# Kernel optimization log

Hardware: AMD Instinct MI355X
Metric: run time of the kernel (lower is better)

Reference implementation:

```python
import jax, jax.numpy as jnp
import numpy as np

KERNEL_MUL = 2.0
KERNEL_NUM = 5


def setup_inputs() -> dict:
    key = jax.random.key(0)
    k1, k2 = jax.random.split(key)
    N, D = 4096, 256
    source = jax.random.normal(k1, (N, D), dtype=jnp.float32)
    target = jax.random.normal(k2, (N, D), dtype=jnp.float32)
    return {"source": source, "target": target}


def _gaussian_kernel_sum(source, target):
    # total: [2N, D]
    total = jnp.concatenate([source, target], axis=0)
    n = total.shape[0]
    sq = jnp.sum(total * total, axis=1)  # [2N]
    L2 = sq[:, None] + sq[None, :] - 2.0 * (total @ total.T)  # [2N, 2N]
    # Bandwidth from detached mean of off-diagonal-normalized sum (torch uses .data)
    bandwidth = jax.lax.stop_gradient(jnp.sum(L2)) / (n * n - n)
    bandwidth = bandwidth / (KERNEL_MUL ** (KERNEL_NUM // 2))
    kernels = sum(
        jnp.exp(-L2 / (bandwidth * (KERNEL_MUL ** i))) for i in range(KERNEL_NUM)
    )
    return kernels


def reference(source, target):
    b = source.shape[0]
    K = _gaussian_kernel_sum(source, target)
    XX = jnp.mean(K[:b, :b])
    YY = jnp.mean(K[b:, b:])
    XY = jnp.mean(K[:b, b:])
    YX = jnp.mean(K[b:, :b])
    return XX + YY - XY - YX
```

## Files before the change

kernel.cpp:

```cpp
#include <hip/hip_runtime.h>


#define NROWS 8192
#define HALF  4096
#define DIM   256
#define CONVB 256
#define NTILE 2080
#define GRIDP 512

typedef float f32x4 __attribute__((ext_vector_type(4)));
typedef float f32x2 __attribute__((ext_vector_type(2)));

__device__ __forceinline__ const float* row_ptr(const float* src, const float* tgt, int r) {
    return (r < HALF) ? (src + (size_t)r * DIM) : (tgt + (size_t)(r - HALF) * DIM);
}

__device__ __forceinline__ void gload_lds16(const void* g, void* l) {
    __builtin_amdgcn_global_load_lds(
        (const __attribute__((address_space(1))) unsigned int*)g,
        (__attribute__((address_space(3))) unsigned int*)l, 16, 0, 0);
}

__device__ __forceinline__ void stage_panel(const ulonglong2* plane, int P,
                                            ulonglong2* lds, int w, int lane) {
    #pragma unroll
    for (int i = 0; i < 8; ++i) {
        int k = w + 4 * i;
        int u = k >> 1;
        int h = k & 1;
        int rg = (h * 64 + lane) ^ ((u & 3) << 1);
        gload_lds16(plane + (size_t)P * 2048 + (size_t)u * 128 + rg,
                    lds + u * 128 + h * 64);
    }
}

__global__ __launch_bounds__(256) void k_conv(const float* __restrict__ src,
                                              const float* __restrict__ tgt,
                                              unsigned char* __restrict__ hi,
                                              float* __restrict__ sq,
                                              float* __restrict__ part,
                                              double* __restrict__ parts1,
                                              float* __restrict__ out) {
    __shared__ __align__(16) unsigned char sh8[32 * 256];
    __shared__ float4 cs[4][64];
    __shared__ double s1s[4];

    int w = threadIdx.x >> 6, lane = threadIdx.x & 63;
    int r0 = blockIdx.x * 32;

    float4 v[8];
    #pragma unroll
    for (int i = 0; i < 8; ++i) {
        int row = r0 + w * 8 + i;
        v[i] = ((const float4*)row_ptr(src, tgt, row))[lane];
    }

    float4 csum = {0.f, 0.f, 0.f, 0.f};
    double s1w = 0.0;
    #pragma unroll
    for (int i = 0; i < 8; ++i) {
        int rl  = w * 8 + i;
        float xs[4] = {v[i].x, v[i].y, v[i].z, v[i].w};
        int pk = __builtin_amdgcn_cvt_pk_fp8_f32(xs[0], xs[1], 0, false);
        pk     = __builtin_amdgcn_cvt_pk_fp8_f32(xs[2], xs[3], pk, true);
        int o  = lane >> 1, h = lane & 1;
        *(int*)&sh8[rl * 256 + (((o ^ rl) & 31) << 3) + (h << 2)] = pk;
        csum.x += xs[0]; csum.y += xs[1]; csum.z += xs[2]; csum.w += xs[3];
        float sf = xs[0]*xs[0] + xs[1]*xs[1] + xs[2]*xs[2] + xs[3]*xs[3];
        float q0 = __builtin_amdgcn_cvt_f32_fp8(pk, 0);
        float q1 = __builtin_amdgcn_cvt_f32_fp8(pk, 1);
        float q2 = __builtin_amdgcn_cvt_f32_fp8(pk, 2);
        float q3 = __builtin_amdgcn_cvt_f32_fp8(pk, 3);
        float sQ = q0*q0 + q1*q1 + q2*q2 + q3*q3;
        #pragma unroll
        for (int off = 32; off; off >>= 1) {
            sf += __shfl_xor(sf, off, 64);
            sQ += __shfl_xor(sQ, off, 64);
        }
        if (lane == 0) { sq[r0 + rl] = sQ; s1w += (double)sf; }
    }
    __syncthreads();
    int panel = blockIdx.x >> 2, quarter = blockIdx.x & 3;
    #pragma unroll
    for (int c = threadIdx.x; c < 512; c += 256) {
        int u = c >> 5, rl = c & 31;
        int tt = u >> 2, j = u & 3;
        int o0 = 8 * tt + j;
        int o1 = 8 * tt + 4 + j;
        unsigned long long q0 = *(const unsigned long long*)
            &sh8[rl * 256 + (((o0 ^ rl) & 31) << 3)];
        unsigned long long q1 = *(const unsigned long long*)
            &sh8[rl * 256 + (((o1 ^ rl) & 31) << 3)];
        ulonglong2 q = {q0, q1};
        size_t goff = ((size_t)panel * 2048 + (size_t)u * 128 + quarter * 32 + rl);
        ((ulonglong2*)hi)[goff] = q;
    }
    cs[w][lane] = csum;
    if (lane == 0) s1s[w] = s1w;
    __syncthreads();
    if (w == 0) {
        float4 a = cs[0][lane], b = cs[1][lane], c = cs[2][lane], d = cs[3][lane];
        float4 tot = {a.x + b.x + c.x + d.x, a.y + b.y + c.y + d.y,
                      a.z + b.z + c.z + d.z, a.w + b.w + c.w + d.w};
        *(float4*)&part[(size_t)blockIdx.x * DIM + lane * 4] = tot;
        if (lane == 0) parts1[blockIdx.x] = s1s[0] + s1s[1] + s1s[2] + s1s[3];
    }
    if (blockIdx.x == 0 && threadIdx.x == 0) out[0] = 0.0f;
}

__global__ __launch_bounds__(256) void k_scale(const double* __restrict__ parts1,
                                               const float* __restrict__ part,
                                               float* __restrict__ scale) {
    __shared__ double sh[256];
    int t = threadIdx.x;
    sh[t] = parts1[t];
    __syncthreads();
    for (int off = 128; off; off >>= 1) {
        if (t < off) sh[t] += sh[t + off];
        __syncthreads();
    }
    double S1 = sh[0];
    __syncthreads();
    float c0 = 0.f, c1 = 0.f, c2 = 0.f, c3 = 0.f;
    #pragma unroll 16
    for (int b = 0; b < CONVB; b += 4) {
        c0 += part[(b + 0) * DIM + t];
        c1 += part[(b + 1) * DIM + t];
        c2 += part[(b + 2) * DIM + t];
        c3 += part[(b + 3) * DIM + t];
    }
    double c = (double)((c0 + c1) + (c2 + c3));
    sh[t] = c * c;
    __syncthreads();
    for (int off = 128; off; off >>= 1) {
        if (t < off) sh[t] += sh[t + off];
        __syncthreads();
    }
    if (t == 0) {
        double S2    = sh[0];
        double n     = (double)NROWS;
        double sumL2 = 2.0 * n * S1 - 2.0 * S2;
        double bw    = sumL2 / (n * n - n) / 4.0;
        *scale = (float)(-1.0 / (16.0 * bw * 0.69314718055994530942));
    }
}

__global__ __launch_bounds__(256, 2) void k_pairs(const unsigned char* __restrict__ hi,
                                                  const float* __restrict__ sq,
                                                  const float* __restrict__ scale_p,
                                                  float* __restrict__ pb) {
    __shared__ __align__(16) ulonglong2 ldsA[2048];
    __shared__ __align__(16) ulonglong2 ldsB[2048];
    __shared__ float wsum[4];

    int bid = blockIdx.x;
    int t0 = (bid * NTILE) / GRIDP;
    int t1 = ((bid + 1) * NTILE) / GRIDP;

    int id = t0, I = 0;
    for (;;) {
        int c = 64 - I;
        if (id < c) break;
        id -= c; ++I;
    }
    int J = I + id;

    int t    = threadIdx.x;
    int lane = t & 63;
    int w    = t >> 6;
    int lr   = lane & 15, lq = lane >> 4;
    int wr   = w >> 1, wc = w & 1;
    int lrx  = lr ^ (lq << 1);

    const ulonglong2* plane = (const ulonglong2*)hi;
    float s = *scale_p;
    f32x2 m2s = {-2.0f * s, -2.0f * s};

    stage_panel(plane, I, ldsA, w, lane);
    if (J != I) stage_panel(plane, J, ldsB, w, lane);
    asm volatile("s_waitcnt vmcnt(0)");
    __syncthreads();

    float wtot = 0.0f;
    int curI = I, curJ = J;

    #pragma unroll 1
    for (int tile = t0; tile < t1; ++tile) {
        const ulonglong2* lB  = (curJ == curI) ? ldsA : ldsB;
        const ulonglong2* pAl = ldsA + lq * 128 + wr * 64 + lrx;
        const ulonglong2* pBl = lB   + lq * 128 + wc * 64 + lrx;

        ulonglong2 fA[4][4], fB[4][4];
        #pragma unroll
        for (int tt = 0; tt < 4; ++tt) {
            #pragma unroll
            for (int m = 0; m < 4; ++m) fA[tt][m] = pAl[tt * 512 + m * 16];
            #pragma unroll
            for (int n = 0; n < 4; ++n) fB[tt][n] = pBl[tt * 512 + n * 16];
        }
        __syncthreads();

        int nI = curI, nJ = curJ + 1;
        if (nJ == 64) { nI = curI + 1; nJ = nI; }
        if (tile + 1 < t1) {
            if (nI != curI) stage_panel(plane, nI, ldsA, w, lane);
            else            stage_panel(plane, nJ, ldsB, w, lane);
        }

        f32x4 acc[4][4];
        #pragma unroll
        for (int m = 0; m < 4; ++m)
            #pragma unroll
            for (int n = 0; n < 4; ++n) acc[m][n] = (f32x4){0.f, 0.f, 0.f, 0.f};
        #pragma unroll
        for (int tt = 0; tt < 4; ++tt) {
            #pragma unroll
            for (int m = 0; m < 4; ++m)
                #pragma unroll
                for (int n = 0; n < 4; ++n)
                    acc[m][n] = __builtin_amdgcn_mfma_f32_16x16x32_fp8_fp8(
                        (long)fA[tt][m].x, (long)fB[tt][n].x, acc[m][n], 0, 0, 0);
            #pragma unroll
            for (int m = 0; m < 4; ++m)
                #pragma unroll
                for (int n = 0; n < 4; ++n)
                    acc[m][n] = __builtin_amdgcn_mfma_f32_16x16x32_fp8_fp8(
                        (long)fA[tt][m].y, (long)fB[tt][n].y, acc[m][n], 0, 0, 0);
        }

        float wgt = (curJ == curI) ? 1.0f : 2.0f;
        float sgn = ((curI < 32) == (curJ < 32)) ? 1.0f : -1.0f;
        int ro_eff = curI * 128 + wr * 64;
        int co_eff = curJ * 128 + wc * 64;
        float4 sqa4[4];
        float  sqbv[4];
        #pragma unroll
        for (int m = 0; m < 4; ++m) sqa4[m] = *(const float4*)&sq[ro_eff + m * 16 + lq * 4];
        #pragma unroll
        for (int n = 0; n < 4; ++n) sqbv[n] = s * sq[co_eff + n * 16 + lr];

        f32x2 ssa01[4], ssa23[4];
        #pragma unroll
        for (int m = 0; m < 4; ++m) {
            ssa01[m] = (f32x2){s * sqa4[m].x, s * sqa4[m].y};
            ssa23[m] = (f32x2){s * sqa4[m].z, s * sqa4[m].w};
        }

        f32x2 acc0 = {0.f, 0.f}, acc1 = {0.f, 0.f};
        #pragma unroll
        for (int m = 0; m < 4; ++m) {
            #pragma unroll
            for (int n = 0; n < 4; ++n) {
                f32x2 sbn = {sqbv[n], sqbv[n]};
                f32x2 a01 = {acc[m][n][0], acc[m][n][1]};
                f32x2 a23 = {acc[m][n][2], acc[m][n][3]};
                f32x2 e01 = (ssa01[m] + sbn) + m2s * a01;
                f32x2 e23 = (ssa23[m] + sbn) + m2s * a23;
                f32x2 u01, u23;
                u01.x = __builtin_amdgcn_exp2f(e01.x);
                u01.y = __builtin_amdgcn_exp2f(e01.y);
                u23.x = __builtin_amdgcn_exp2f(e23.x);
                u23.y = __builtin_amdgcn_exp2f(e23.y);
                f32x2 p2a = u01 * u01, p4a = p2a * p2a, p8a = p4a * p4a, p16a = p8a * p8a;
                f32x2 p2b = u23 * u23, p4b = p2b * p2b, p8b = p4b * p4b, p16b = p8b * p8b;
                acc0 += ((u01 + p2a) + (p4a + p8a)) + p16a;
                acc1 += ((u23 + p2b) + (p4b + p8b)) + p16b;
            }
        }
        wtot += ((acc0.x + acc0.y) + (acc1.x + acc1.y)) * sgn * wgt;

        asm volatile("s_waitcnt vmcnt(0)");
        __syncthreads();
        curI = nI; curJ = nJ;
    }

    #pragma unroll
    for (int off = 32; off; off >>= 1) wtot += __shfl_xor(wtot, off, 64);
    if (lane == 0) wsum[w] = wtot;
    __syncthreads();
    if (t == 0) {
        float tot = wsum[0] + wsum[1] + wsum[2] + wsum[3];
        pb[blockIdx.x] = tot * (1.0f / ((float)HALF * (float)HALF));
    }
}

__global__ __launch_bounds__(256) void k_fin(const float* __restrict__ pb,
                                             float* __restrict__ out) {
    __shared__ float sh[4];
    int t = threadIdx.x, lane = t & 63, w = t >> 6;
    float s = 0.f;
    for (int i = t; i < GRIDP; i += 256) s += pb[i];
    #pragma unroll
    for (int off = 32; off; off >>= 1) s += __shfl_xor(s, off, 64);
    if (lane == 0) sh[w] = s;
    __syncthreads();
    if (t == 0) out[0] = sh[0] + sh[1] + sh[2] + sh[3];
}

extern "C" void kernel_launch(void* const* d_in, const int* in_sizes, int n_in,
                              void* d_out, int out_size, void* d_ws, size_t ws_size,
                              hipStream_t stream) {
    const float* src = (const float*)d_in[0];
    const float* tgt = (const float*)d_in[1];
    float* out = (float*)d_out;

    char* ws = (char*)d_ws;
    float*  scale  = (float*)(ws + 16);
    float*  sq     = (float*)(ws + 64);
    float*  part   = (float*)(ws + 64 + 32768);
    double* parts1 = (double*)(ws + 64 + 32768 + 262144);
    unsigned char* hi = (unsigned char*)(ws + 297024);
    float*  pb     = (float*)(ws + 2394176);

    k_conv <<<CONVB, 256, 0, stream>>>(src, tgt, hi, sq, part, parts1, out);
    k_scale<<<1, 256, 0, stream>>>(parts1, part, scale);
    k_pairs<<<GRIDP, 256, 0, stream>>>(hi, sq, scale, pb);
    k_fin  <<<1, 256, 0, stream>>>(pb, out);
}
```

Before: 96.35 us.

## Fold scale and final reduction kernels into pair kernel, cutting launches to two

Removes the single-block scale kernel by having every pair block redundantly reduce the per-block partial sums and compute the bandwidth scale itself, overlapped with the initial panel staging loads. Also removes the final reduction kernel by accumulating block results with atomics into eight slots, plus a completion counter so the last block writes the output. This saves two launch gaps and their serial single-block phases. In exchange each of the 512 blocks re-reads about 256 KB of partials and adds LDS use and reduction barriers before its main loop.

```diff
diff --git a/kernel.cpp b/kernel.cpp
--- a/kernel.cpp
+++ b/kernel.cpp
@@ -40,6 +40,8 @@
                                               float* __restrict__ sq,
                                               float* __restrict__ part,
                                               double* __restrict__ parts1,
+                                              float* __restrict__ outacc,
+                                              unsigned int* __restrict__ cnt,
                                               float* __restrict__ out) {
     __shared__ __align__(16) unsigned char sh8[32 * 256];
     __shared__ float4 cs[4][64];
@@ -53,6 +55,11 @@
     for (int i = 0; i < 8; ++i) {
         int row = r0 + w * 8 + i;
         v[i] = ((const float4*)row_ptr(src, tgt, row))[lane];
+    }
+
+    if (blockIdx.x == 0) {
+        if (threadIdx.x < 8) outacc[threadIdx.x] = 0.0f;
+        if (threadIdx.x == 0) { *cnt = 0u; out[0] = 0.0f; }
     }
 
     float4 csum = {0.f, 0.f, 0.f, 0.f};
@@ -105,53 +112,19 @@
         *(float4*)&part[(size_t)blockIdx.x * DIM + lane * 4] = tot;
         if (lane == 0) parts1[blockIdx.x] = s1s[0] + s1s[1] + s1s[2] + s1s[3];
     }
-    if (blockIdx.x == 0 && threadIdx.x == 0) out[0] = 0.0f;
-}
-
-__global__ __launch_bounds__(256) void k_scale(const double* __restrict__ parts1,
-                                               const float* __restrict__ part,
-                                               float* __restrict__ scale) {
-    __shared__ double sh[256];
-    int t = threadIdx.x;
-    sh[t] = parts1[t];
-    __syncthreads();
-    for (int off = 128; off; off >>= 1) {
-        if (t < off) sh[t] += sh[t + off];
-        __syncthreads();
-    }
-    double S1 = sh[0];
-    __syncthreads();
-    float c0 = 0.f, c1 = 0.f, c2 = 0.f, c3 = 0.f;
-    #pragma unroll 16
-    for (int b = 0; b < CONVB; b += 4) {
-        c0 += part[(b + 0) * DIM + t];
-        c1 += part[(b + 1) * DIM + t];
-        c2 += part[(b + 2) * DIM + t];
-        c3 += part[(b + 3) * DIM + t];
-    }
-    double c = (double)((c0 + c1) + (c2 + c3));
-    sh[t] = c * c;
-    __syncthreads();
-    for (int off = 128; off; off >>= 1) {
-        if (t < off) sh[t] += sh[t + off];
-        __syncthreads();
-    }
-    if (t == 0) {
-        double S2    = sh[0];
-        double n     = (double)NROWS;
-        double sumL2 = 2.0 * n * S1 - 2.0 * S2;
-        double bw    = sumL2 / (n * n - n) / 4.0;
-        *scale = (float)(-1.0 / (16.0 * bw * 0.69314718055994530942));
-    }
 }
 
 __global__ __launch_bounds__(256, 2) void k_pairs(const unsigned char* __restrict__ hi,
                                                   const float* __restrict__ sq,
-                                                  const float* __restrict__ scale_p,
-                                                  float* __restrict__ pb) {
+                                                  const float* __restrict__ part,
+                                                  const double* __restrict__ parts1,
+                                                  float* __restrict__ outacc,
+                                                  unsigned int* __restrict__ cnt,
+                                                  float* __restrict__ out) {
     __shared__ __align__(16) ulonglong2 ldsA[2048];
     __shared__ __align__(16) ulonglong2 ldsB[2048];
     __shared__ float wsum[4];
+    __shared__ double shd[256];
 
     int bid = blockIdx.x;
     int t0 = (bid * NTILE) / GRIDP;
@@ -173,11 +146,42 @@
     int lrx  = lr ^ (lq << 1);
 
     const ulonglong2* plane = (const ulonglong2*)hi;
-    float s = *scale_p;
-    f32x2 m2s = {-2.0f * s, -2.0f * s};
 
     stage_panel(plane, I, ldsA, w, lane);
     if (J != I) stage_panel(plane, J, ldsB, w, lane);
+
+    shd[t] = parts1[t];
+    __syncthreads();
+    for (int off = 128; off; off >>= 1) {
+        if (t < off) shd[t] += shd[t + off];
+        __syncthreads();
+    }
+    double S1 = shd[0];
+    __syncthreads();
+    {
+        float c0 = 0.f, c1 = 0.f, c2 = 0.f, c3 = 0.f;
+        #pragma unroll 16
+        for (int b = 0; b < CONVB; b += 4) {
+            c0 += part[(b + 0) * DIM + t];
+            c1 += part[(b + 1) * DIM + t];
+            c2 += part[(b + 2) * DIM + t];
+            c3 += part[(b + 3) * DIM + t];
+        }
+        double c = (double)((c0 + c1) + (c2 + c3));
+        shd[t] = c * c;
+    }
+    __syncthreads();
+    for (int off = 128; off; off >>= 1) {
+        if (t < off) shd[t] += shd[t + off];
+        __syncthreads();
+    }
+    double S2    = shd[0];
+    double nd    = (double)NROWS;
+    double sumL2 = 2.0 * nd * S1 - 2.0 * S2;
+    double bw    = sumL2 / (nd * nd - nd) / 4.0;
+    float  s     = (float)(-1.0 / (16.0 * bw * 0.69314718055994530942));
+    f32x2  m2s   = {-2.0f * s, -2.0f * s};
+
     asm volatile("s_waitcnt vmcnt(0)");
     __syncthreads();
 
@@ -279,22 +283,18 @@
     if (lane == 0) wsum[w] = wtot;
     __syncthreads();
     if (t == 0) {
-        float tot = wsum[0] + wsum[1] + wsum[2] + wsum[3];
-        pb[blockIdx.x] = tot * (1.0f / ((float)HALF * (float)HALF));
-    }
-}
-
-__global__ __launch_bounds__(256) void k_fin(const float* __restrict__ pb,
-                                             float* __restrict__ out) {
-    __shared__ float sh[4];
-    int t = threadIdx.x, lane = t & 63, w = t >> 6;
-    float s = 0.f;
-    for (int i = t; i < GRIDP; i += 256) s += pb[i];
-    #pragma unroll
-    for (int off = 32; off; off >>= 1) s += __shfl_xor(s, off, 64);
-    if (lane == 0) sh[w] = s;
-    __syncthreads();
-    if (t == 0) out[0] = sh[0] + sh[1] + sh[2] + sh[3];
+        float tot = (wsum[0] + wsum[1] + wsum[2] + wsum[3])
+                  * (1.0f / ((float)HALF * (float)HALF));
+        float r = atomicAdd(&outacc[bid & 7], tot);
+        asm volatile("" :: "v"(r) : "memory");
+        unsigned prev = atomicAdd(cnt, 1u);
+        if (prev == (unsigned)(GRIDP - 1)) {
+            float total = 0.0f;
+            #pragma unroll
+            for (int k2 = 0; k2 < 8; ++k2) total += atomicAdd(&outacc[k2], 0.0f);
+            out[0] = total;
+        }
+    }
 }
 
 extern "C" void kernel_launch(void* const* d_in, const int* in_sizes, int n_in,
@@ -305,15 +305,14 @@
     float* out = (float*)d_out;
 
     char* ws = (char*)d_ws;
-    float*  scale  = (float*)(ws + 16);
-    float*  sq     = (float*)(ws + 64);
-    float*  part   = (float*)(ws + 64 + 32768);
-    double* parts1 = (double*)(ws + 64 + 32768 + 262144);
-    unsigned char* hi = (unsigned char*)(ws + 297024);
-    float*  pb     = (float*)(ws + 2394176);
-
-    k_conv <<<CONVB, 256, 0, stream>>>(src, tgt, hi, sq, part, parts1, out);
-    k_scale<<<1, 256, 0, stream>>>(parts1, part, scale);
-    k_pairs<<<GRIDP, 256, 0, stream>>>(hi, sq, scale, pb);
-    k_fin  <<<1, 256, 0, stream>>>(pb, out);
-}
+    unsigned int* cnt = (unsigned int*)(ws + 0);
+    float*  outacc = (float*)(ws + 64);
+    float*  sq     = (float*)(ws + 128);
+    float*  part   = (float*)(ws + 33024);
+    double* parts1 = (double*)(ws + 295424);
+    unsigned char* hi = (unsigned char*)(ws + 297472);
+
+    k_conv <<<CONVB, 256, 0, stream>>>(src, tgt, hi, sq, part, parts1,
+                                       outacc, cnt, out);
+    k_pairs<<<GRIDP, 256, 0, stream>>>(hi, sq, part, parts1, outacc, cnt, out);
+}
```

Measured after the change: 96.40 us. No clear change (+0.1%).
